# Optimization experiments

Hardware: AMD Instinct MI355X
Metric: run time of the kernel (lower is better)

Reference implementation:

```python
import jax, jax.numpy as jnp
import numpy as np
from jax import lax

# Config mirroring __init__ defaults
TEMP = 0.1           # temperature (constant schedule; set_epoch never called)
KSIZE = 11           # dilation_kernel_size
MAX_POS = 2048       # max_pos_per_image
NEG_RATIO = 5.0      # neg_pos_ratio
EPS = 1e-8
KN = int(NEG_RATIO * MAX_POS)   # max negatives per image (10240)
KC = 2 * KN                      # rim candidate pool for hard mining (20480)


def _forward(features, labels):
    B, C, H, W = features.shape
    HW = H * W
    fg = labels > 0                                   # (B,H,W)
    # Dilate foreground via max-pool (kernel KSIZE, stride 1, SAME) -> rim band
    dil = lax.reduce_window(fg.astype(jnp.float32), -jnp.inf, lax.max,
                            (1, KSIZE, KSIZE), (1, 1, 1), 'SAME') > 0
    rim = dil & (~fg)
    # L2-normalized per-pixel features, (B,HW,C)
    f = features.reshape(B, C, HW).transpose(0, 2, 1)
    f = f / jnp.maximum(jnp.linalg.norm(f, axis=-1, keepdims=True), EPS)
    fg_flat = fg.reshape(B, HW)
    rim_flat = rim.reshape(B, HW)
    rank = jnp.arange(HW, dtype=jnp.float32) / HW     # deterministic tiebreak

    def per_image(fi, fgi, rimi):
        # --- sample positives (deterministic raster-order selection of fg pixels) ---
        _, pidx = lax.top_k(fgi.astype(jnp.float32) * 2.0 - rank, MAX_POS)
        vp = fgi[pidx]                                # valid-positive mask (P,)
        pf = fi[pidx]                                 # (P,C)
        # --- rim candidate pool ---
        _, cidx = lax.top_k(rimi.astype(jnp.float32) * 2.0 - rank, KC)
        vc = rimi[cidx]
        cf = fi[cidx]                                 # (KC,C)
        # --- hard negative mining: negatives most similar to any positive ---
        sim = pf @ cf.T                               # (P,KC)
        max_sim = jnp.max(jnp.where(vp[:, None], sim, -jnp.inf), axis=0)
        nvals, nsel = lax.top_k(jnp.where(vc, max_sim, -jnp.inf), KN)
        n_allowed = jnp.minimum(jnp.floor(NEG_RATIO * jnp.sum(vp)), KN)
        vn = jnp.isfinite(nvals) & (jnp.arange(KN) < n_allowed)
        nf = cf[nsel]                                 # (KN,C)
        # --- contrastive loss: positives attract, rim negatives repel ---
        lpp = (pf @ pf.T) / TEMP                      # (P,P)
        lpn = (pf @ nf.T) / TEMP                      # (P,KN)
        eye = jnp.eye(MAX_POS, dtype=bool)
        mpp = vp[:, None] & vp[None, :] & (~eye)
        mpn = vp[:, None] & vn[None, :]
        NEGC = jnp.float32(-1e30)
        all_logits = jnp.concatenate([jnp.where(mpp, lpp, NEGC),
                                      jnp.where(mpn, lpn, NEGC)], axis=1)
        denom = jax.nn.logsumexp(all_logits, axis=1)  # (P,)
        npairs = jnp.sum(mpp, axis=1)
        li = -jnp.sum(jnp.where(mpp, lpp - denom[:, None], 0.0), axis=1) \
             / jnp.maximum(npairs, 1)
        av = vp & (npairs > 0)
        img_loss = jnp.sum(jnp.where(av, li, 0.0)) / jnp.maximum(jnp.sum(av), 1)
        return img_loss, jnp.any(av)

    losses, has = jax.vmap(per_image)(f, fg_flat, rim_flat)
    return jnp.sum(jnp.where(has, losses, 0.0)) / jnp.maximum(jnp.sum(has), 1)


def setup_inputs() -> dict:
    key = jax.random.key(0)
    k1, k2 = jax.random.split(key)
    features = jax.random.normal(k1, (4, 64, 384, 384), dtype=jnp.float32)
    labels = jax.random.randint(k2, (4, 384, 384), 0, 2).astype(jnp.int64)
    return {"features": features, "labels": labels}


def reference(features, labels):
    return _forward(features, labels)
```

## Files before the change

### kernel.cpp

```cpp
#include <hip/hip_runtime.h>
#include <hip/hip_bf16.h>

#define DEVI __device__ __forceinline__

static constexpr int cB = 4, cC = 64, cH = 384, cW = 384;
static constexpr int cHW = cH * cW;
static constexpr int cP  = 2048;
static constexpr int cKC = 20480;
static constexpr int cKN = 10240;
static constexpr int cNT = cP + cKN;
static constexpr float cTEMP_INV = 10.0f;
static constexpr int cCHUNK = 2048;
static constexpr int cNB = cHW / cCHUNK;
static constexpr int cNCH = 8;
static constexpr int cTPC = (cNT / 16) / cNCH;

using f32x4  = __attribute__((ext_vector_type(4))) float;
using bf16x8 = __attribute__((ext_vector_type(8))) __bf16;

static constexpr size_t off_fg   = 0;
static constexpr size_t off_tmp  = off_fg   + (size_t)cB * cHW;
static constexpr size_t off_rim  = off_tmp  + (size_t)cB * cHW;
static constexpr size_t off_pidx = off_rim  + (size_t)cB * cHW;
static constexpr size_t off_cidx = off_pidx + (size_t)cB * cP * 4;
static constexpr size_t off_scal = off_cidx + (size_t)cB * cKC * 4;
static constexpr size_t off_EL   = off_scal + 256;
static constexpr size_t off_msim = off_EL   + (size_t)cNCH * cB * cP * 8;
static constexpr size_t off_nsel = off_msim + (size_t)cB * 2 * cKC * 4;
static constexpr size_t off_G    = off_nsel + (size_t)cB * cKN * 4;
static constexpr size_t off_cf   = off_G    + (size_t)cB * cNT * cC * 2;
static constexpr size_t off_bcnt = off_cf   + (size_t)cB * cKC * cC * 2;
static constexpr size_t off_boff = off_bcnt + (size_t)cB * cNB * 4;

DEVI f32x4 mfma16(bf16x8 a, bf16x8 b, f32x4 c) {
  return __builtin_amdgcn_mfma_f32_16x16x32_bf16(a, b, c, 0, 0, 0);
}

__global__ __launch_bounds__(256) void k_fg_hdil(const int* labels, unsigned char* fg, unsigned char* tmp) {
  int t = blockIdx.x * 256 + threadIdx.x;
  int base = t * 8;
  int x0 = base % cW;
  const int* lb = labels + (base - x0);
  unsigned m = 0;
#pragma unroll
  for (int j = 0; j < 18; j++) {
    int x = x0 - 5 + j;
    int v = (x >= 0 && x < cW) ? (lb[x] > 0) : 0;
    m |= (unsigned)v << j;
  }
  unsigned long long fgb = 0, tmb = 0;
#pragma unroll
  for (int e = 0; e < 8; e++) {
    fgb |= (unsigned long long)((m >> (e + 5)) & 1u) << (8 * e);
    tmb |= (unsigned long long)(((m >> e) & 0x7FFu) ? 1u : 0u) << (8 * e);
  }
  *(unsigned long long*)(fg + base)  = fgb;
  *(unsigned long long*)(tmp + base) = tmb;
}

__global__ __launch_bounds__(256) void k_vdil_count(const unsigned char* tmp, const unsigned char* fg,
                                                    unsigned char* rim, int* blkcnt) {
  __shared__ int red[256];
  int b = blockIdx.y, blk = blockIdx.x, tid = threadIdx.x;
  int base = blk * cCHUNK + tid * 8;
  const unsigned char* tb  = tmp + (size_t)b * cHW;
  const unsigned char* fgb = fg  + (size_t)b * cHW;
  unsigned long long fv = *(const unsigned long long*)(fgb + base);
  int y = base / cW, x = base % cW;
  int lo = max(y - 5, 0), hi = min(y + 5, cH - 1);
  unsigned long long m8 = 0;
  for (int yy = lo; yy <= hi; yy++) m8 |= *(const unsigned long long*)(tb + yy * cW + x);
  unsigned long long pk = m8 & (fv ^ 0x0101010101010101ULL);
  *(unsigned long long*)(rim + (size_t)b * cHW + base) = pk;
  int cfg  = __popcll(fv & 0x0101010101010101ULL);
  int crim = __popcll(pk & 0x0101010101010101ULL);
  red[tid] = cfg | (crim << 16);
  __syncthreads();
  for (int s = 128; s > 0; s >>= 1) {
    if (tid < s) red[tid] += red[tid + s];
    __syncthreads();
  }
  if (tid == 0) blkcnt[b * cNB + blk] = red[0];
}

__global__ __launch_bounds__(128) void k_offsets(const int* blkcnt, int2* blkoff, int* scal) {
  __shared__ int sf[128], sr[128];
  int b = blockIdx.x, tid = threadIdx.x;
  int v = (tid < cNB) ? blkcnt[b * cNB + tid] : 0;
  int f = v & 0xffff, r = v >> 16;
  sf[tid] = f; sr[tid] = r;
  __syncthreads();
  for (int d = 1; d < 128; d <<= 1) {
    int tf = (tid >= d) ? sf[tid - d] : 0;
    int tr = (tid >= d) ? sr[tid - d] : 0;
    __syncthreads();
    sf[tid] += tf; sr[tid] += tr;
    __syncthreads();
  }
  if (tid < cNB) blkoff[b * cNB + tid] = make_int2(sf[tid] - f, sr[tid] - r);
  if (tid == 0) {
    int nfg = sf[cNB - 1], nrim = sr[cNB - 1];
    scal[b * 16 + 0] = nfg;
    scal[b * 16 + 1] = min(nfg, cP);
    scal[b * 16 + 2] = min(nrim, cKC);
    scal[b * 16 + 4] = nrim;
  }
}

__device__ int scan_excl_256(int v, int* lds) {
  int tid = threadIdx.x;
  lds[tid] = v;
  __syncthreads();
  for (int d = 1; d < 256; d <<= 1) {
    int t = (tid >= d) ? lds[tid - d] : 0;
    __syncthreads();
    lds[tid] += t;
    __syncthreads();
  }
  int e = lds[tid] - v;
  __syncthreads();
  return e;
}

__global__ __launch_bounds__(256) void k_scatter(const unsigned char* fg, const unsigned char* rim,
                                                 const int2* blkoff, const int* scal,
                                                 int* pidx, int* cidx) {
  __shared__ int lds[256];
  int b = blockIdx.y, blk = blockIdx.x, tid = threadIdx.x;
  int2 off = blkoff[b * cNB + blk];
  int nfg  = scal[b * 16 + 0];
  int nrim = scal[b * 16 + 4];
  bool needf = (off.x < cP)  || (nfg  < cP);
  bool needr = (off.y < cKC) || (nrim < cKC);
  if (!needf && !needr) return;
  int base = blk * cCHUNK + tid * 8;
  const unsigned char* fgb  = fg  + (size_t)b * cHW;
  const unsigned char* rimb = rim + (size_t)b * cHW;
  unsigned long long fv = *(const unsigned long long*)(fgb + base);
  unsigned long long rv = *(const unsigned long long*)(rimb + base);
  int cfg  = __popcll(fv & 0x0101010101010101ULL);
  int crim = __popcll(rv & 0x0101010101010101ULL);
  int ex = scan_excl_256(cfg | (crim << 16), lds);
  int of  = off.x + (ex & 0xffff);
  int orr = off.y + (ex >> 16);
  int* pout = pidx + (size_t)b * cP;
  int* cout = cidx + (size_t)b * cKC;
#pragma unroll
  for (int e = 0; e < 8; e++) {
    int p = base + e;
    int f = (int)((fv >> (8 * e)) & 1);
    int r = (int)((rv >> (8 * e)) & 1);
    if (f) { if (of < cP) pout[of] = p; of++; }
    else if (nfg < cP) { int o = nfg + (p - of); if (o < cP) pout[o] = p; }
    if (r) { if (orr < cKC) cout[orr] = p; orr++; }
    else if (nrim < cKC) { int o = nrim + (p - orr); if (o < cKC) cout[o] = p; }
  }
}

__global__ __launch_bounds__(256) void k_gather_norm(const float* feat, const int* pidx, const int* cidx,
                                                     __hip_bfloat16* G, __hip_bfloat16* cf) {
  int b = blockIdx.y;
  int bx = blockIdx.x;
  int p;
  __hip_bfloat16* out;
  if (bx < cP / 256) {
    int i = bx * 256 + threadIdx.x;
    p = pidx[(size_t)b * cP + i];
    out = G + (size_t)b * cNT * cC + (size_t)i * cC;
  } else {
    int i = (bx - cP / 256) * 256 + threadIdx.x;
    p = cidx[(size_t)b * cKC + i];
    out = cf + (size_t)b * cKC * cC + (size_t)i * cC;
  }
  const float* fb = feat + (size_t)b * cC * cHW + p;
  float v[cC];
  float ss = 0.f;
#pragma unroll
  for (int c = 0; c < cC; c++) { float t = fb[(size_t)c * cHW]; v[c] = t; ss += t * t; }
  float sc = 1.0f / fmaxf(sqrtf(ss), 1e-8f);
#pragma unroll
  for (int c = 0; c < cC; c++) out[c] = __float2bfloat16(v[c] * sc);
}

__global__ __launch_bounds__(256) void k_mine(const __hip_bfloat16* G, const __hip_bfloat16* cf,
                                              const int* scal, float* msim) {
  int b = blockIdx.z, rc = blockIdx.y;
  int P_valid = scal[b * 16 + 1];
  int wave = threadIdx.x >> 6, lane = threadIdx.x & 63;
  int lr = lane & 15, quad = lane >> 4;
  int colbase = (blockIdx.x * 4 + wave) * 128;
  float* msout = msim + ((size_t)b * 2 + rc) * cKC;
  int mt0 = rc * 64;
  int chunk_lo = mt0 * 16;
  if (chunk_lo >= P_valid) {
    if (quad == 0) {
#pragma unroll
      for (int tt = 0; tt < 8; tt++) msout[colbase + tt * 16 + lr] = -INFINITY;
    }
    return;
  }
  bool chunk_full = (chunk_lo + 1024) <= P_valid;
  const __bf16* pf  = (const __bf16*)(G  + (size_t)b * cNT * cC);
  const __bf16* cfb = (const __bf16*)(cf + (size_t)b * cKC * cC);

  bf16x8 bfr[8][2];
#pragma unroll
  for (int tt = 0; tt < 8; tt++) {
    const __bf16* src = cfb + (size_t)(colbase + tt * 16 + lr) * cC + quad * 8;
    bfr[tt][0] = *(const bf16x8*)src;
    bfr[tt][1] = *(const bf16x8*)(src + 32);
  }
  float cmax[8];
#pragma unroll
  for (int tt = 0; tt < 8; tt++) cmax[tt] = -INFINITY;

  const __bf16* ap = pf + (size_t)(mt0 * 16 + lr) * cC + quad * 8;
  bf16x8 a0 = *(const bf16x8*)ap;
  bf16x8 a1 = *(const bf16x8*)(ap + 32);
  for (int mt = mt0; mt < mt0 + 64; mt++) {
    int nmt = min(mt + 1, mt0 + 63);
    const __bf16* np = pf + (size_t)(nmt * 16 + lr) * cC + quad * 8;
    bf16x8 na0 = *(const bf16x8*)np;
    bf16x8 na1 = *(const bf16x8*)(np + 32);
    int rb = mt * 16 + quad * 4;
#pragma unroll
    for (int tt = 0; tt < 8; tt++) {
      f32x4 acc = {0, 0, 0, 0};
      acc = mfma16(a0, bfr[tt][0], acc);
      acc = mfma16(a1, bfr[tt][1], acc);
      if (chunk_full) {
        cmax[tt] = fmaxf(cmax[tt], fmaxf(fmaxf(acc[0], acc[1]), fmaxf(acc[2], acc[3])));
      } else {
#pragma unroll
        for (int r = 0; r < 4; r++)
          cmax[tt] = fmaxf(cmax[tt], (rb + r) < P_valid ? acc[r] : -INFINITY);
      }
    }
    a0 = na0; a1 = na1;
  }
#pragma unroll
  for (int tt = 0; tt < 8; tt++) {
    float c = cmax[tt];
    c = fmaxf(c, __shfl_xor(c, 16));
    c = fmaxf(c, __shfl_xor(c, 32));
    cmax[tt] = c;
  }
  if (quad == 0) {
#pragma unroll
    for (int tt = 0; tt < 8; tt++) msout[colbase + tt * 16 + lr] = cmax[tt];
  }
}

DEVI unsigned f2key(float f) {
  unsigned u = __float_as_uint(f);
  return (u & 0x80000000u) ? ~u : (u | 0x80000000u);
}

__device__ int scan_excl_1024(int v, int* lds, int* total) {
  int tid = threadIdx.x;
  lds[tid] = v;
  __syncthreads();
  for (int d = 1; d < 1024; d <<= 1) {
    int t = (tid >= d) ? lds[tid - d] : 0;
    __syncthreads();
    lds[tid] += t;
    __syncthreads();
  }
  *total = lds[1023];
  int e = lds[tid] - v;
  __syncthreads();
  return e;
}

__global__ __launch_bounds__(1024) void k_selneg(const float* msim, int* nsel, int* scal) {
  __shared__ int hist[256];
  __shared__ int suf[256];
  __shared__ int lds[1024];
  __shared__ unsigned sh_prefix;
  __shared__ int sh_rem;
  int b = blockIdx.x, tid = threadIdx.x;
  const float* ms0 = msim + ((size_t)b * 2 + 0) * cKC;
  const float* ms1 = msim + ((size_t)b * 2 + 1) * cKC;
  int P_valid = scal[b * 16 + 1], C_valid = scal[b * 16 + 2];
  int n_allowed = min(5 * P_valid, cKN);
  int nfin = (P_valid > 0) ? C_valid : 0;
  int KEEP = min(n_allowed, nfin);
  if (tid == 0) scal[b * 16 + 3] = KEEP;
  if (KEEP == 0) return;

  unsigned prefix = 0;
  int remaining = KEEP;
  for (int shift = 24; shift >= 0; shift -= 8) {
    if (tid < 256) hist[tid] = 0;
    __syncthreads();
    for (int c = tid; c < cKC; c += 1024) {
      unsigned key = (c < C_valid) ? f2key(fmaxf(ms0[c], ms1[c])) : 0u;
      if (shift == 24 || (key >> (shift + 8)) == prefix)
        atomicAdd(&hist[(key >> shift) & 255], 1);
    }
    __syncthreads();
    if (tid < 256) suf[tid] = hist[tid];
    __syncthreads();
    for (int d = 1; d < 256; d <<= 1) {
      int t = (tid < 256 && tid + d < 256) ? suf[tid + d] : 0;
      __syncthreads();
      if (tid < 256) suf[tid] += t;
      __syncthreads();
    }
    if (tid < 256) {
      int s = suf[tid];
      int sn = (tid < 255) ? suf[tid + 1] : 0;
      if (s >= remaining && sn < remaining) {
        sh_prefix = (prefix << 8) | (unsigned)tid;
        sh_rem = remaining - sn;
      }
    }
    __syncthreads();
    prefix = sh_prefix; remaining = sh_rem;
    __syncthreads();
  }
  unsigned T = prefix;

  const int CH2 = cKC / 1024;
  int s = tid * CH2;
  unsigned keys[CH2];
  int cntA = 0, cntT = 0;
  for (int e = 0; e < CH2; e++) {
    int c = s + e;
    unsigned key = (c < C_valid) ? f2key(fmaxf(ms0[c], ms1[c])) : 0u;
    keys[e] = key;
    cntA += (key > T);
    cntT += (key == T);
  }
  int totA, totT;
  int offA = scan_excl_1024(cntA, lds, &totA);
  int offT = scan_excl_1024(cntT, lds, &totT);
  int* out = nsel + (size_t)b * cKN;
  int oa = offA, ot = offT;
  for (int e = 0; e < CH2; e++) {
    unsigned key = keys[e];
    if (key > T) { out[oa++] = s + e; }
    else if (key == T) { if (ot < remaining) out[totA + ot] = s + e; ot++; }
  }
}

__global__ __launch_bounds__(256) void k_gather_neg(const __hip_bfloat16* cf, const int* nsel,
                                                    const int* scal, __hip_bfloat16* G) {
  int b = blockIdx.y;
  int KEEP = scal[b * 16 + 3];
  int t = blockIdx.x * 256 + threadIdx.x;
  int k = t >> 3, part = t & 7;
  if (k >= cKN) return;
  int4 val = {0, 0, 0, 0};
  if (k < KEEP) {
    int src = nsel[(size_t)b * cKN + k];
    val = *(const int4*)((const __bf16*)(cf + (size_t)b * cKC * cC) + (size_t)src * cC + part * 8);
  }
  *(int4*)((__bf16*)(G + (size_t)b * cNT * cC) + (size_t)(cP + k) * cC + part * 8) = val;
}

__global__ __launch_bounds__(256) void k_loss_part(const __hip_bfloat16* G, const int* scal, float2* ELp) {
  __shared__ float sE[4][64];
  __shared__ float sL[4][64];
  int b = blockIdx.z, chunk = blockIdx.y;
  int P_valid = scal[b * 16 + 1];
  int KEEP = scal[b * 16 + 3];
  if (P_valid < 2) return;
  int wave = threadIdx.x >> 6, lane = threadIdx.x & 63;
  int lr = lane & 15, quad = lane >> 4;
  int rowbase = blockIdx.x * 64;
  const __bf16* Gb = (const __bf16*)G + (size_t)b * cNT * cC;

  bf16x8 afr[4][2];
#pragma unroll
  for (int rt = 0; rt < 4; rt++) {
    const __bf16* src = Gb + (size_t)(rowbase + rt * 16 + lr) * cC + quad * 8;
    afr[rt][0] = *(const bf16x8*)src;
    afr[rt][1] = *(const bf16x8*)(src + 32);
  }
  float eacc[4][4] = {};
  float lacc[4][4] = {};
  int ct0 = chunk * cTPC;
  for (int ct = ct0 + wave; ct < ct0 + cTPC; ct += 4) {
    int tb = ct * 16;
    bool is_pos = tb < cP;
    int vlimit = is_pos ? P_valid : (cP + KEEP);
    if (tb >= vlimit) continue;
    bool all_valid = (tb + 16) <= vlimit;
    bool has_diag = is_pos && (tb >= rowbase) && (tb < rowbase + 64);
    const __bf16* bsrc = Gb + (size_t)(tb + lr) * cC + quad * 8;
    bf16x8 b0 = *(const bf16x8*)bsrc;
    bf16x8 b1 = *(const bf16x8*)(bsrc + 32);
    f32x4 acc[4];
#pragma unroll
    for (int rt = 0; rt < 4; rt++) {
      f32x4 a = {0, 0, 0, 0};
      a = mfma16(afr[rt][0], b0, a);
      a = mfma16(afr[rt][1], b1, a);
      acc[rt] = a;
    }
    if (all_valid && !has_diag) {
      if (is_pos) {
#pragma unroll
        for (int rt = 0; rt < 4; rt++)
#pragma unroll
          for (int r = 0; r < 4; r++) {
            float logit = acc[rt][r] * cTEMP_INV;
            eacc[rt][r] += __expf(logit);
            lacc[rt][r] += logit;
          }
      } else {
#pragma unroll
        for (int rt = 0; rt < 4; rt++)
#pragma unroll
          for (int r = 0; r < 4; r++)
            eacc[rt][r] += __expf(acc[rt][r] * cTEMP_INV);
      }
    } else {
      bool colv = (tb + lr) < vlimit;
#pragma unroll
      for (int rt = 0; rt < 4; rt++) {
        int rb = rowbase + rt * 16 + quad * 4;
#pragma unroll
        for (int r = 0; r < 4; r++) {
          float logit = acc[rt][r] * cTEMP_INV;
          bool use = colv && !(has_diag && (tb + lr) == (rb + r));
          float e = __expf(logit);
          eacc[rt][r] += use ? e : 0.0f;
          if (is_pos) lacc[rt][r] += use ? logit : 0.0f;
        }
      }
    }
  }
#pragma unroll
  for (int rt = 0; rt < 4; rt++) {
#pragma unroll
    for (int r = 0; r < 4; r++) {
      float e = eacc[rt][r], l = lacc[rt][r];
#pragma unroll
      for (int d = 1; d < 16; d <<= 1) {
        e += __shfl_xor(e, d);
        l += __shfl_xor(l, d);
      }
      if (lr == 0) {
        sE[wave][rt * 16 + quad * 4 + r] = e;
        sL[wave][rt * 16 + quad * 4 + r] = l;
      }
    }
  }
  __syncthreads();
  if (threadIdx.x < 64) {
    int row = rowbase + threadIdx.x;
    float E = sE[0][threadIdx.x] + sE[1][threadIdx.x] + sE[2][threadIdx.x] + sE[3][threadIdx.x];
    float L = sL[0][threadIdx.x] + sL[1][threadIdx.x] + sL[2][threadIdx.x] + sL[3][threadIdx.x];
    ELp[((size_t)chunk * cB + b) * cP + row] = make_float2(E, L);
  }
}

__global__ __launch_bounds__(1024) void k_loss_fin(const int* scal, const float2* ELp, float* out) {
  __shared__ float ssum[16];
  int tid = threadIdx.x;
  int b = tid >> 8, t = tid & 255;
  int Pv = scal[b * 16 + 1];
  float s = 0.f;
  if (Pv >= 2) {
    float inv = 1.0f / (float)(Pv - 1);
#pragma unroll
    for (int e = 0; e < 8; e++) {
      int row = t * 8 + e;
      if (row < Pv) {
        float E = 0.f, L = 0.f;
#pragma unroll
        for (int ch = 0; ch < cNCH; ch++) {
          float2 el = ELp[((size_t)ch * cB + b) * cP + row];
          E += el.x; L += el.y;
        }
        s += logf(E) - L * inv;
      }
    }
  }
#pragma unroll
  for (int d = 1; d < 64; d <<= 1) s += __shfl_xor(s, d);
  if ((tid & 63) == 0) ssum[tid >> 6] = s;
  __syncthreads();
  if (tid == 0) {
    float tot = 0.f;
    int cnt = 0;
    for (int bb = 0; bb < cB; bb++) {
      int P = scal[bb * 16 + 1];
      if (P >= 2) {
        float is = ssum[bb * 4] + ssum[bb * 4 + 1] + ssum[bb * 4 + 2] + ssum[bb * 4 + 3];
        tot += is / (float)P;
        cnt++;
      }
    }
    out[0] = tot / (float)(cnt > 0 ? cnt : 1);
  }
}

extern "C" void kernel_launch(void* const* d_in, const int* in_sizes, int n_in,
                              void* d_out, int out_size, void* d_ws, size_t ws_size,
                              hipStream_t stream) {
  const float* feat = (const float*)d_in[0];
  const int* labels = (const int*)d_in[1];
  char* ws = (char*)d_ws;
  unsigned char* fg  = (unsigned char*)(ws + off_fg);
  unsigned char* tmp = (unsigned char*)(ws + off_tmp);
  unsigned char* rim = (unsigned char*)(ws + off_rim);
  int* pidx = (int*)(ws + off_pidx);
  int* cidx = (int*)(ws + off_cidx);
  int* scal = (int*)(ws + off_scal);
  float2* ELp = (float2*)(ws + off_EL);
  float* msim = (float*)(ws + off_msim);
  int* nsel = (int*)(ws + off_nsel);
  __hip_bfloat16* G  = (__hip_bfloat16*)(ws + off_G);
  __hip_bfloat16* cf = (__hip_bfloat16*)(ws + off_cf);
  int* blkcnt = (int*)(ws + off_bcnt);
  int2* blkoff = (int2*)(ws + off_boff);
  float* out = (float*)d_out;

  k_fg_hdil<<<cB * cHW / 8 / 256, 256, 0, stream>>>(labels, fg, tmp);
  k_vdil_count<<<dim3(cNB, cB), 256, 0, stream>>>(tmp, fg, rim, blkcnt);
  k_offsets<<<cB, 128, 0, stream>>>(blkcnt, blkoff, scal);
  k_scatter<<<dim3(cNB, cB), 256, 0, stream>>>(fg, rim, blkoff, scal, pidx, cidx);
  k_gather_norm<<<dim3(cP / 256 + cKC / 256, cB), 256, 0, stream>>>(feat, pidx, cidx, G, cf);
  k_mine<<<dim3(cKC / 512, 2, cB), 256, 0, stream>>>(G, cf, scal, msim);
  k_selneg<<<cB, 1024, 0, stream>>>(msim, nsel, scal);
  k_gather_neg<<<dim3(cKN * 8 / 256, cB), 256, 0, stream>>>(cf, nsel, scal, G);
  k_loss_part<<<dim3(cP / 64, cNCH, cB), 256, 0, stream>>>(G, scal, ELp);
  k_loss_fin<<<1, 1024, 0, stream>>>(scal, ELp, out);
}
```

Measured before the change: 370.0 us.

## Stage positives in LDS for mining, gather negatives inline, fuse loss finalization

The mining kernel now stages the positive tile in swizzled shared memory and gives each wave 10 column tiles instead of 8, which reduces the grid. Negative selection caches its keys in registers once rather than recomputing them on every radix pass. The separate negative-gather kernel is removed: the loss kernel reads negative rows indirectly through nsel from the candidate pool, and a last-block atomic counter folds in the final reduction, so two launches and a buffer round trip go away. In exchange, B-operand loads in the loss become indirect and scattered, and the final reduction now runs on a single 256-thread block.

```diff
diff --git a/kernel.cpp b/kernel.cpp
--- a/kernel.cpp
+++ b/kernel.cpp
@@ -14,6 +14,10 @@
 static constexpr int cNB = cHW / cCHUNK;
 static constexpr int cNCH = 8;
 static constexpr int cTPC = (cNT / 16) / cNCH;
+static constexpr int cMTW = 10;
+static constexpr int cMCW = 160;
+static constexpr int cMCB = 640;
+static constexpr int cLOSS_BLOCKS = (cP / 64) * cNCH * cB;
 
 using f32x4  = __attribute__((ext_vector_type(4))) float;
 using bf16x8 = __attribute__((ext_vector_type(8))) __bf16;
@@ -28,7 +32,7 @@
 static constexpr size_t off_msim = off_EL   + (size_t)cNCH * cB * cP * 8;
 static constexpr size_t off_nsel = off_msim + (size_t)cB * 2 * cKC * 4;
 static constexpr size_t off_G    = off_nsel + (size_t)cB * cKN * 4;
-static constexpr size_t off_cf   = off_G    + (size_t)cB * cNT * cC * 2;
+static constexpr size_t off_cf   = off_G    + (size_t)cB * cP * cC * 2;
 static constexpr size_t off_bcnt = off_cf   + (size_t)cB * cKC * cC * 2;
 static constexpr size_t off_boff = off_bcnt + (size_t)cB * cNB * 4;
 
@@ -86,6 +90,7 @@
 __global__ __launch_bounds__(128) void k_offsets(const int* blkcnt, int2* blkoff, int* scal) {
   __shared__ int sf[128], sr[128];
   int b = blockIdx.x, tid = threadIdx.x;
+  if (b == 0 && tid == 0) scal[15] = 0;
   int v = (tid < cNB) ? blkcnt[b * cNB + tid] : 0;
   int f = v & 0xffff, r = v >> 16;
   sf[tid] = f; sr[tid] = r;
@@ -166,7 +171,7 @@
   if (bx < cP / 256) {
     int i = bx * 256 + threadIdx.x;
     p = pidx[(size_t)b * cP + i];
-    out = G + (size_t)b * cNT * cC + (size_t)i * cC;
+    out = G + (size_t)b * cP * cC + (size_t)i * cC;
   } else {
     int i = (bx - cP / 256) * 256 + threadIdx.x;
     p = cidx[(size_t)b * cKC + i];
@@ -184,70 +189,72 @@
 
 __global__ __launch_bounds__(256) void k_mine(const __hip_bfloat16* G, const __hip_bfloat16* cf,
                                               const int* scal, float* msim) {
+  __shared__ int4 smem[4096];
   int b = blockIdx.z, rc = blockIdx.y;
   int P_valid = scal[b * 16 + 1];
   int wave = threadIdx.x >> 6, lane = threadIdx.x & 63;
   int lr = lane & 15, quad = lane >> 4;
-  int colbase = (blockIdx.x * 4 + wave) * 128;
+  int colbase = blockIdx.x * cMCB + wave * cMCW;
   float* msout = msim + ((size_t)b * 2 + rc) * cKC;
-  int mt0 = rc * 64;
-  int chunk_lo = mt0 * 16;
+  int chunk_lo = rc * 1024;
   if (chunk_lo >= P_valid) {
     if (quad == 0) {
 #pragma unroll
-      for (int tt = 0; tt < 8; tt++) msout[colbase + tt * 16 + lr] = -INFINITY;
+      for (int tt = 0; tt < cMTW; tt++) msout[colbase + tt * 16 + lr] = -INFINITY;
     }
     return;
   }
-  bool chunk_full = (chunk_lo + 1024) <= P_valid;
-  const __bf16* pf  = (const __bf16*)(G  + (size_t)b * cNT * cC);
+  const int4* pf4 = (const int4*)((const __bf16*)(G + (size_t)b * cP * cC)) + (size_t)chunk_lo * 8;
   const __bf16* cfb = (const __bf16*)(cf + (size_t)b * cKC * cC);
 
-  bf16x8 bfr[8][2];
-#pragma unroll
-  for (int tt = 0; tt < 8; tt++) {
+  bf16x8 bfr[cMTW][2];
+#pragma unroll
+  for (int tt = 0; tt < cMTW; tt++) {
     const __bf16* src = cfb + (size_t)(colbase + tt * 16 + lr) * cC + quad * 8;
     bfr[tt][0] = *(const bf16x8*)src;
     bfr[tt][1] = *(const bf16x8*)(src + 32);
   }
-  float cmax[8];
-#pragma unroll
-  for (int tt = 0; tt < 8; tt++) cmax[tt] = -INFINITY;
-
-  const __bf16* ap = pf + (size_t)(mt0 * 16 + lr) * cC + quad * 8;
-  bf16x8 a0 = *(const bf16x8*)ap;
-  bf16x8 a1 = *(const bf16x8*)(ap + 32);
-  for (int mt = mt0; mt < mt0 + 64; mt++) {
-    int nmt = min(mt + 1, mt0 + 63);
-    const __bf16* np = pf + (size_t)(nmt * 16 + lr) * cC + quad * 8;
-    bf16x8 na0 = *(const bf16x8*)np;
-    bf16x8 na1 = *(const bf16x8*)(np + 32);
-    int rb = mt * 16 + quad * 4;
-#pragma unroll
-    for (int tt = 0; tt < 8; tt++) {
-      f32x4 acc = {0, 0, 0, 0};
-      acc = mfma16(a0, bfr[tt][0], acc);
-      acc = mfma16(a1, bfr[tt][1], acc);
-      if (chunk_full) {
-        cmax[tt] = fmaxf(cmax[tt], fmaxf(fmaxf(acc[0], acc[1]), fmaxf(acc[2], acc[3])));
-      } else {
-#pragma unroll
-        for (int r = 0; r < 4; r++)
-          cmax[tt] = fmaxf(cmax[tt], (rb + r) < P_valid ? acc[r] : -INFINITY);
-      }
-    }
-    a0 = na0; a1 = na1;
-  }
-#pragma unroll
-  for (int tt = 0; tt < 8; tt++) {
+  float cmax[cMTW];
+#pragma unroll
+  for (int tt = 0; tt < cMTW; tt++) cmax[tt] = -INFINITY;
+
+  int swz  = quad ^ (lr & 7);
+  int swz2 = (quad + 4) ^ (lr & 7);
+  for (int half = 0; half < 2; half++) {
+    for (int i = threadIdx.x; i < 4096; i += 256) {
+      int r = i >> 3, q = i & 7;
+      smem[r * 8 + (q ^ (r & 7))] = pf4[(size_t)(half * 512 + r) * 8 + q];
+    }
+    __syncthreads();
+    int rowg0 = chunk_lo + half * 512;
+    bool full = (rowg0 + 512) <= P_valid;
+    for (int mtl = 0; mtl < 32; mtl++) {
+      int rl = mtl * 16 + lr;
+      bf16x8 a0 = *(bf16x8*)&smem[rl * 8 + swz];
+      bf16x8 a1 = *(bf16x8*)&smem[rl * 8 + swz2];
+      int rb = rowg0 + mtl * 16 + quad * 4;
+#pragma unroll
+      for (int tt = 0; tt < cMTW; tt++) {
+        f32x4 acc = {0, 0, 0, 0};
+        acc = mfma16(a0, bfr[tt][0], acc);
+        acc = mfma16(a1, bfr[tt][1], acc);
+        if (full) {
+          cmax[tt] = fmaxf(cmax[tt], fmaxf(fmaxf(acc[0], acc[1]), fmaxf(acc[2], acc[3])));
+        } else {
+#pragma unroll
+          for (int r = 0; r < 4; r++)
+            cmax[tt] = fmaxf(cmax[tt], (rb + r) < P_valid ? acc[r] : -INFINITY);
+        }
+      }
+    }
+    __syncthreads();
+  }
+#pragma unroll
+  for (int tt = 0; tt < cMTW; tt++) {
     float c = cmax[tt];
     c = fmaxf(c, __shfl_xor(c, 16));
     c = fmaxf(c, __shfl_xor(c, 32));
-    cmax[tt] = c;
-  }
-  if (quad == 0) {
-#pragma unroll
-    for (int tt = 0; tt < 8; tt++) msout[colbase + tt * 16 + lr] = cmax[tt];
+    if (quad == 0) msout[colbase + tt * 16 + lr] = c;
   }
 }
 
@@ -288,13 +295,23 @@
   if (tid == 0) scal[b * 16 + 3] = KEEP;
   if (KEEP == 0) return;
 
+  const int CH2 = cKC / 1024;
+  int base = tid * CH2;
+  unsigned keys[CH2];
+#pragma unroll
+  for (int e = 0; e < CH2; e++) {
+    int c = base + e;
+    keys[e] = (c < C_valid) ? f2key(fmaxf(ms0[c], ms1[c])) : 0u;
+  }
+
   unsigned prefix = 0;
   int remaining = KEEP;
   for (int shift = 24; shift >= 0; shift -= 8) {
     if (tid < 256) hist[tid] = 0;
     __syncthreads();
-    for (int c = tid; c < cKC; c += 1024) {
-      unsigned key = (c < C_valid) ? f2key(fmaxf(ms0[c], ms1[c])) : 0u;
+#pragma unroll
+    for (int e = 0; e < CH2; e++) {
+      unsigned key = keys[e];
       if (shift == 24 || (key >> (shift + 8)) == prefix)
         atomicAdd(&hist[(key >> shift) & 255], 1);
     }
@@ -321,16 +338,11 @@
   }
   unsigned T = prefix;
 
-  const int CH2 = cKC / 1024;
-  int s = tid * CH2;
-  unsigned keys[CH2];
   int cntA = 0, cntT = 0;
+#pragma unroll
   for (int e = 0; e < CH2; e++) {
-    int c = s + e;
-    unsigned key = (c < C_valid) ? f2key(fmaxf(ms0[c], ms1[c])) : 0u;
-    keys[e] = key;
-    cntA += (key > T);
-    cntT += (key == T);
+    cntA += (keys[e] > T);
+    cntT += (keys[e] == T);
   }
   int totA, totT;
   int offA = scan_excl_1024(cntA, lds, &totA);
@@ -339,163 +351,157 @@
   int oa = offA, ot = offT;
   for (int e = 0; e < CH2; e++) {
     unsigned key = keys[e];
-    if (key > T) { out[oa++] = s + e; }
-    else if (key == T) { if (ot < remaining) out[totA + ot] = s + e; ot++; }
-  }
-}
-
-__global__ __launch_bounds__(256) void k_gather_neg(const __hip_bfloat16* cf, const int* nsel,
-                                                    const int* scal, __hip_bfloat16* G) {
-  int b = blockIdx.y;
-  int KEEP = scal[b * 16 + 3];
-  int t = blockIdx.x * 256 + threadIdx.x;
-  int k = t >> 3, part = t & 7;
-  if (k >= cKN) return;
-  int4 val = {0, 0, 0, 0};
-  if (k < KEEP) {
-    int src = nsel[(size_t)b * cKN + k];
-    val = *(const int4*)((const __bf16*)(cf + (size_t)b * cKC * cC) + (size_t)src * cC + part * 8);
-  }
-  *(int4*)((__bf16*)(G + (size_t)b * cNT * cC) + (size_t)(cP + k) * cC + part * 8) = val;
-}
-
-__global__ __launch_bounds__(256) void k_loss_part(const __hip_bfloat16* G, const int* scal, float2* ELp) {
+    if (key > T) { out[oa++] = base + e; }
+    else if (key == T) { if (ot < remaining) out[totA + ot] = base + e; ot++; }
+  }
+}
+
+__global__ __launch_bounds__(256) void k_loss(const __hip_bfloat16* G, const __hip_bfloat16* cf,
+                                              const int* nsel, int* scal, float2* ELp, float* out) {
   __shared__ float sE[4][64];
   __shared__ float sL[4][64];
+  __shared__ int sIsLast;
+  __shared__ float sred[4];
   int b = blockIdx.z, chunk = blockIdx.y;
   int P_valid = scal[b * 16 + 1];
   int KEEP = scal[b * 16 + 3];
-  if (P_valid < 2) return;
   int wave = threadIdx.x >> 6, lane = threadIdx.x & 63;
   int lr = lane & 15, quad = lane >> 4;
   int rowbase = blockIdx.x * 64;
-  const __bf16* Gb = (const __bf16*)G + (size_t)b * cNT * cC;
-
-  bf16x8 afr[4][2];
-#pragma unroll
-  for (int rt = 0; rt < 4; rt++) {
-    const __bf16* src = Gb + (size_t)(rowbase + rt * 16 + lr) * cC + quad * 8;
-    afr[rt][0] = *(const bf16x8*)src;
-    afr[rt][1] = *(const bf16x8*)(src + 32);
-  }
-  float eacc[4][4] = {};
-  float lacc[4][4] = {};
-  int ct0 = chunk * cTPC;
-  for (int ct = ct0 + wave; ct < ct0 + cTPC; ct += 4) {
-    int tb = ct * 16;
-    bool is_pos = tb < cP;
-    int vlimit = is_pos ? P_valid : (cP + KEEP);
-    if (tb >= vlimit) continue;
-    bool all_valid = (tb + 16) <= vlimit;
-    bool has_diag = is_pos && (tb >= rowbase) && (tb < rowbase + 64);
-    const __bf16* bsrc = Gb + (size_t)(tb + lr) * cC + quad * 8;
-    bf16x8 b0 = *(const bf16x8*)bsrc;
-    bf16x8 b1 = *(const bf16x8*)(bsrc + 32);
-    f32x4 acc[4];
+  const __bf16* Gb  = (const __bf16*)G  + (size_t)b * cP * cC;
+  const __bf16* cfb = (const __bf16*)cf + (size_t)b * cKC * cC;
+  const int* nselb = nsel + (size_t)b * cKN;
+
+  if (P_valid >= 2) {
+    bf16x8 afr[4][2];
 #pragma unroll
     for (int rt = 0; rt < 4; rt++) {
-      f32x4 a = {0, 0, 0, 0};
-      a = mfma16(afr[rt][0], b0, a);
-      a = mfma16(afr[rt][1], b1, a);
-      acc[rt] = a;
-    }
-    if (all_valid && !has_diag) {
+      const __bf16* src = Gb + (size_t)(rowbase + rt * 16 + lr) * cC + quad * 8;
+      afr[rt][0] = *(const bf16x8*)src;
+      afr[rt][1] = *(const bf16x8*)(src + 32);
+    }
+    float eacc[4][4] = {};
+    float lacc[4][4] = {};
+    int ct0 = chunk * cTPC;
+    for (int ct = ct0 + wave; ct < ct0 + cTPC; ct += 4) {
+      int tb = ct * 16;
+      bool is_pos = tb < cP;
+      int vlimit = is_pos ? P_valid : (cP + KEEP);
+      if (tb >= vlimit) continue;
+      bool all_valid = (tb + 16) <= vlimit;
+      bool has_diag = is_pos && (tb >= rowbase) && (tb < rowbase + 64);
+      const __bf16* bsrc;
       if (is_pos) {
-#pragma unroll
-        for (int rt = 0; rt < 4; rt++)
+        bsrc = Gb + (size_t)(tb + lr) * cC + quad * 8;
+      } else {
+        int k = tb - cP + lr;
+        int kk = min(k, KEEP - 1);
+        int idx = nselb[kk];
+        bsrc = cfb + (size_t)idx * cC + quad * 8;
+      }
+      bf16x8 b0 = *(const bf16x8*)bsrc;
+      bf16x8 b1 = *(const bf16x8*)(bsrc + 32);
+      f32x4 acc[4];
+#pragma unroll
+      for (int rt = 0; rt < 4; rt++) {
+        f32x4 a = {0, 0, 0, 0};
+        a = mfma16(afr[rt][0], b0, a);
+        a = mfma16(afr[rt][1], b1, a);
+        acc[rt] = a;
+      }
+      if (all_valid && !has_diag) {
+        if (is_pos) {
+#pragma unroll
+          for (int rt = 0; rt < 4; rt++)
+#pragma unroll
+            for (int r = 0; r < 4; r++) {
+              float logit = acc[rt][r] * cTEMP_INV;
+              eacc[rt][r] += __expf(logit);
+              lacc[rt][r] += logit;
+            }
+        } else {
+#pragma unroll
+          for (int rt = 0; rt < 4; rt++)
+#pragma unroll
+            for (int r = 0; r < 4; r++)
+              eacc[rt][r] += __expf(acc[rt][r] * cTEMP_INV);
+        }
+      } else {
+        bool colv = (tb + lr) < vlimit;
+#pragma unroll
+        for (int rt = 0; rt < 4; rt++) {
+          int rb = rowbase + rt * 16 + quad * 4;
 #pragma unroll
           for (int r = 0; r < 4; r++) {
             float logit = acc[rt][r] * cTEMP_INV;
-            eacc[rt][r] += __expf(logit);
-            lacc[rt][r] += logit;
+            bool use = colv && !(has_diag && (tb + lr) == (rb + r));
+            float e = __expf(logit);
+            eacc[rt][r] += use ? e : 0.0f;
+            if (is_pos) lacc[rt][r] += use ? logit : 0.0f;
           }
-      } else {
-#pragma unroll
-        for (int rt = 0; rt < 4; rt++)
-#pragma unroll
-          for (int r = 0; r < 4; r++)
-            eacc[rt][r] += __expf(acc[rt][r] * cTEMP_INV);
-      }
-    } else {
-      bool colv = (tb + lr) < vlimit;
-#pragma unroll
-      for (int rt = 0; rt < 4; rt++) {
-        int rb = rowbase + rt * 16 + quad * 4;
-#pragma unroll
-        for (int r = 0; r < 4; r++) {
-          float logit = acc[rt][r] * cTEMP_INV;
-          bool use = colv && !(has_diag && (tb + lr) == (rb + r));
-          float e = __expf(logit);
-          eacc[rt][r] += use ? e : 0.0f;
-          if (is_pos) lacc[rt][r] += use ? logit : 0.0f;
         }
       }
     }
-  }
-#pragma unroll
-  for (int rt = 0; rt < 4; rt++) {
-#pragma unroll
-    for (int r = 0; r < 4; r++) {
-      float e = eacc[rt][r], l = lacc[rt][r];
-#pragma unroll
-      for (int d = 1; d < 16; d <<= 1) {
-        e += __shfl_xor(e, d);
-        l += __shfl_xor(l, d);
-      }
-      if (lr == 0) {
-        sE[wave][rt * 16 + quad * 4 + r] = e;
-        sL[wave][rt * 16 + quad * 4 + r] = l;
-      }
-    }
-  }
-  __syncthreads();
-  if (threadIdx.x < 64) {
-    int row = rowbase + threadIdx.x;
-    float E = sE[0][threadIdx.x] + sE[1][threadIdx.x] + sE[2][threadIdx.x] + sE[3][threadIdx.x];
-    float L = sL[0][threadIdx.x] + sL[1][threadIdx.x] + sL[2][threadIdx.x] + sL[3][threadIdx.x];
-    ELp[((size_t)chunk * cB + b) * cP + row] = make_float2(E, L);
-  }
-}
-
-__global__ __launch_bounds__(1024) void k_loss_fin(const int* scal, const float2* ELp, float* out) {
-  __shared__ float ssum[16];
-  int tid = threadIdx.x;
-  int b = tid >> 8, t = tid & 255;
-  int Pv = scal[b * 16 + 1];
-  float s = 0.f;
-  if (Pv >= 2) {
+#pragma unroll
+    for (int rt = 0; rt < 4; rt++) {
+#pragma unroll
+      for (int r = 0; r < 4; r++) {
+        float e = eacc[rt][r], l = lacc[rt][r];
+#pragma unroll
+        for (int d = 1; d < 16; d <<= 1) {
+          e += __shfl_xor(e, d);
+          l += __shfl_xor(l, d);
+        }
+        if (lr == 0) {
+          sE[wave][rt * 16 + quad * 4 + r] = e;
+          sL[wave][rt * 16 + quad * 4 + r] = l;
+        }
+      }
+    }
+    __syncthreads();
+    if (threadIdx.x < 64) {
+      int row = rowbase + threadIdx.x;
+      float E = sE[0][threadIdx.x] + sE[1][threadIdx.x] + sE[2][threadIdx.x] + sE[3][threadIdx.x];
+      float L = sL[0][threadIdx.x] + sL[1][threadIdx.x] + sL[2][threadIdx.x] + sL[3][threadIdx.x];
+      ELp[((size_t)chunk * cB + b) * cP + row] = make_float2(E, L);
+    }
+  }
+
+  __threadfence();
+  if (threadIdx.x == 0) sIsLast = (atomicAdd(&scal[15], 1) == cLOSS_BLOCKS - 1) ? 1 : 0;
+  __syncthreads();
+  if (!sIsLast) return;
+  __threadfence();
+
+  float tot = 0.f;
+  int cnt = 0;
+  for (int bb = 0; bb < cB; bb++) {
+    int Pv = scal[bb * 16 + 1];
+    if (Pv < 2) continue;
     float inv = 1.0f / (float)(Pv - 1);
-#pragma unroll
-    for (int e = 0; e < 8; e++) {
-      int row = t * 8 + e;
+    float s = 0.f;
+    for (int row = threadIdx.x; row < cP; row += 256) {
       if (row < Pv) {
         float E = 0.f, L = 0.f;
 #pragma unroll
         for (int ch = 0; ch < cNCH; ch++) {
-          float2 el = ELp[((size_t)ch * cB + b) * cP + row];
+          float2 el = ELp[((size_t)ch * cB + bb) * cP + row];
           E += el.x; L += el.y;
         }
         s += logf(E) - L * inv;
       }
     }
-  }
-#pragma unroll
-  for (int d = 1; d < 64; d <<= 1) s += __shfl_xor(s, d);
-  if ((tid & 63) == 0) ssum[tid >> 6] = s;
-  __syncthreads();
-  if (tid == 0) {
-    float tot = 0.f;
-    int cnt = 0;
-    for (int bb = 0; bb < cB; bb++) {
-      int P = scal[bb * 16 + 1];
-      if (P >= 2) {
-        float is = ssum[bb * 4] + ssum[bb * 4 + 1] + ssum[bb * 4 + 2] + ssum[bb * 4 + 3];
-        tot += is / (float)P;
-        cnt++;
-      }
-    }
-    out[0] = tot / (float)(cnt > 0 ? cnt : 1);
-  }
+#pragma unroll
+    for (int d = 1; d < 64; d <<= 1) s += __shfl_xor(s, d);
+    __syncthreads();
+    if ((threadIdx.x & 63) == 0) sred[threadIdx.x >> 6] = s;
+    __syncthreads();
+    if (threadIdx.x == 0) {
+      tot += (sred[0] + sred[1] + sred[2] + sred[3]) / (float)Pv;
+      cnt++;
+    }
+  }
+  if (threadIdx.x == 0) out[0] = tot / (float)(cnt > 0 ? cnt : 1);
 }
 
 extern "C" void kernel_launch(void* const* d_in, const int* in_sizes, int n_in,
@@ -524,9 +530,7 @@
   k_offsets<<<cB, 128, 0, stream>>>(blkcnt, blkoff, scal);
   k_scatter<<<dim3(cNB, cB), 256, 0, stream>>>(fg, rim, blkoff, scal, pidx, cidx);
   k_gather_norm<<<dim3(cP / 256 + cKC / 256, cB), 256, 0, stream>>>(feat, pidx, cidx, G, cf);
-  k_mine<<<dim3(cKC / 512, 2, cB), 256, 0, stream>>>(G, cf, scal, msim);
+  k_mine<<<dim3(cKC / cMCB, 2, cB), 256, 0, stream>>>(G, cf, scal, msim);
   k_selneg<<<cB, 1024, 0, stream>>>(msim, nsel, scal);
-  k_gather_neg<<<dim3(cKN * 8 / 256, cB), 256, 0, stream>>>(cf, nsel, scal, G);
-  k_loss_part<<<dim3(cP / 64, cNCH, cB), 256, 0, stream>>>(G, scal, ELp);
-  k_loss_fin<<<1, 1024, 0, stream>>>(scal, ELp, out);
-}
+  k_loss<<<dim3(cP / 64, cNCH, cB), 256, 0, stream>>>(G, cf, nsel, scal, ELp, out);
+}
```

Result: slower. 438.5 us (+18.5%).
